# Kernel tuning notes

Measured on AMD Instinct MI355X. Metric: run time of the kernel, lower is better.

The kernel has to match this reference:

```python
import jax, jax.numpy as jnp
import numpy as np
import math
from jax import lax

B = 128; T = 1024; ENC = 768; H = 256; NMEL = 400
DC = 8; DK = 21; SK = 21; PL = 11

def _prior_np():
    # betabinom.pmf(arange(11), 10, 0.1, 0.9), then flipped (as in torch buffer)
    n = PL - 1; a = 0.1; b = 0.9; lg = math.lgamma
    lp = [lg(n + 1) - lg(k + 1) - lg(n - k + 1) + lg(k + a) + lg(n - k + b) - lg(n + a + b) + lg(a + b) - lg(a) - lg(b) for k in range(PL)]
    return np.exp(np.array(lp, dtype=np.float64))[::-1].copy().astype(np.float32)

def _gru(x, h, wih, whh, bih, bhh):
    # torch GRUCell gate order: r, z, n
    gi = x @ wih.T + bih
    gh = h @ whh.T + bhh
    ir, iz, inn = jnp.split(gi, 3, axis=-1)
    hr, hz, hn = jnp.split(gh, 3, axis=-1)
    r = jax.nn.sigmoid(ir + hr)
    z = jax.nn.sigmoid(iz + hz)
    n = jnp.tanh(inn + r * hn)
    return (1.0 - z) * n + z * h

def _dca(s, alpha, Ww, Wb, Vw, Fk, Uw, Tw, Tb, vw, P):
    Bn, Tn = alpha.shape
    dn = ('NCH', 'OIH', 'NCH')
    # causal prior convolution with flipped beta-binomial pmf
    ap = jnp.pad(alpha[:, None, :], ((0, 0), (0, 0), (PL - 1, 0)))
    p = lax.conv_general_dilated(ap, P.reshape(1, 1, PL), (1,), 'VALID', dimension_numbers=dn)[:, 0, :]
    p = jnp.log(jnp.clip(p, 1e-6))
    # dynamic filters: one [DC, DK] kernel per batch element
    G = jnp.tanh(s @ Ww.T + Wb) @ Vw.T            # [B, DC*DK]
    gk = G.reshape(Bn * DC, 1, DK)
    pad = (DK - 1) // 2
    g = lax.conv_general_dilated(alpha[None, :, :], gk, (1,), [(pad, pad)], dimension_numbers=dn, feature_group_count=Bn)
    g = g.reshape(Bn, DC, Tn).transpose(0, 2, 1)  # [B, T, DC]
    spad = (SK - 1) // 2
    f = lax.conv_general_dilated(alpha[:, None, :], Fk, (1,), [(spad, spad)], dimension_numbers=dn).transpose(0, 2, 1)  # [B, T, SC]
    e = (jnp.tanh(f @ Uw.T + g @ Tw.T + Tb) @ vw.T)[..., 0] + p
    return jax.nn.softmax(e, axis=-1)

def setup_inputs() -> dict:
    key = jax.random.key(0)
    ks = jax.random.split(key, 32)
    s = 0.05
    def nrm(k, shape, sc=s):
        return jax.random.normal(k, shape, dtype=jnp.float32) * sc
    a0 = jax.random.uniform(ks[0], (B, T), dtype=jnp.float32)
    prev_attention = a0 / jnp.sum(a0, axis=-1, keepdims=True)
    return {
        'encoder_outputs': nrm(ks[1], (B, T, ENC), 1.0),
        'prev_frame': nrm(ks[2], (B, NMEL), 1.0),
        'prev_attention': prev_attention,
        'decoder_cell_state': nrm(ks[3], (B, ENC), 1.0),
        'h_att': nrm(ks[4], (B, H), 1.0),
        'h1': nrm(ks[5], (B, H), 1.0),
        'h2': nrm(ks[6], (B, H), 1.0),
        'pre_w1': nrm(ks[7], (H, NMEL)), 'pre_b1': jnp.zeros((H,), jnp.float32),
        'pre_w2': nrm(ks[8], (H // 2, H)), 'pre_b2': jnp.zeros((H // 2,), jnp.float32),
        'dca_Ww': nrm(ks[9], (128, H)), 'dca_Wb': jnp.zeros((128,), jnp.float32),
        'dca_Vw': nrm(ks[10], (DC * DK, 128)),
        'dca_Fk': nrm(ks[11], (DC, 1, SK)),
        'dca_Uw': nrm(ks[12], (128, DC)),
        'dca_Tw': nrm(ks[13], (128, DC)), 'dca_Tb': jnp.zeros((128,), jnp.float32),
        'dca_vw': nrm(ks[14], (1, 128)),
        'att_wih': nrm(ks[15], (3 * H, ENC + H // 2)), 'att_whh': nrm(ks[16], (3 * H, H)),
        'att_bih': jnp.zeros((3 * H,), jnp.float32), 'att_bhh': jnp.zeros((3 * H,), jnp.float32),
        'lin_w': nrm(ks[17], (H, ENC + H)), 'lin_b': jnp.zeros((H,), jnp.float32),
        'r1_wih': nrm(ks[18], (3 * H, H)), 'r1_whh': nrm(ks[19], (3 * H, H)),
        'r1_bih': jnp.zeros((3 * H,), jnp.float32), 'r1_bhh': jnp.zeros((3 * H,), jnp.float32),
        'r2_wih': nrm(ks[20], (3 * H, H)), 'r2_whh': nrm(ks[21], (3 * H, H)),
        'r2_bih': jnp.zeros((3 * H,), jnp.float32), 'r2_bhh': jnp.zeros((3 * H,), jnp.float32),
        'proj_w': nrm(ks[22], (NMEL, H)), 'proj_b': jnp.zeros((NMEL,), jnp.float32),
        'P': jnp.asarray(_prior_np()),
    }

def reference(encoder_outputs, prev_frame, prev_attention, decoder_cell_state, h_att, h1, h2, pre_w1, pre_b1, pre_w2, pre_b2, dca_Ww, dca_Wb, dca_Vw, dca_Fk, dca_Uw, dca_Tw, dca_Tb, dca_vw, att_wih, att_whh, att_bih, att_bhh, lin_w, lin_b, r1_wih, r1_whh, r1_bih, r1_bhh, r2_wih, r2_whh, r2_bih, r2_bhh, proj_w, proj_b, P):
    # pre-net (eval: dropout = identity)
    o = jax.nn.relu(prev_frame @ pre_w1.T + pre_b1)
    o = jax.nn.relu(o @ pre_w2.T + pre_b2)
    h_att_n = _gru(jnp.concatenate([decoder_cell_state, o], axis=-1), h_att, att_wih, att_whh, att_bih, att_bhh)
    alpha = _dca(h_att_n, prev_attention, dca_Ww, dca_Wb, dca_Vw, dca_Fk, dca_Uw, dca_Tw, dca_Tb, dca_vw, P)
    dcs = jnp.einsum('bt,bte->be', alpha, encoder_outputs)
    x = jnp.concatenate([dcs, h_att_n], axis=-1) @ lin_w.T + lin_b
    h1n = _gru(x, h1, r1_wih, r1_whh, r1_bih, r1_bhh)
    x = x + h1n
    h2n = _gru(x, h2, r2_wih, r2_whh, r2_bih, r2_bhh)
    x = x + h2n
    out = (x @ proj_w.T + proj_b).reshape(-1, 80, 5)
    return (out, alpha, dcs, h_att_n, h1n, h2n)
```

## Files before the change

### kernel.cpp

```cpp
#include <hip/hip_runtime.h>

typedef unsigned short u16;
typedef unsigned int u32;

#define NB   128
#define NT   1024
#define NENC 768
#define NH   256
#define NMELS 400

constexpr int OFF_FLAG  = 0;
constexpr int OFF_HATTN = 16;
constexpr int OFF_G     = OFF_HATTN + NB*NH;
constexpr int OFF_ALPHA = OFF_G + NB*168;
constexpr int OFF_DCS   = OFF_ALPHA + NB*NT;
constexpr int OFF_UT    = OFF_DCS + NB*NENC;
constexpr int OFF_TBF   = OFF_UT + 2048;
constexpr int OFF_VWF   = OFF_TBF + 128;
constexpr int OFF_FKF   = OFF_VWF + 128;
constexpr int OFF_PF    = OFF_FKF + 168;

constexpr int OUT_MEL   = 0;
constexpr int OUT_ALPHA = OUT_MEL + NB*NMELS;
constexpr int OUT_DCS   = OUT_ALPHA + NB*NT;
constexpr int OUT_HATT  = OUT_DCS + NB*NENC;
constexpr int OUT_H1    = OUT_HATT + NB*NH;
constexpr int OUT_H2    = OUT_H1 + NB*NH;

__device__ __forceinline__ float bfd(u16 u){ u32 x = ((u32)u) << 16; return __builtin_bit_cast(float, x); }
__device__ __forceinline__ float bflo(u32 u){ return __builtin_bit_cast(float, u << 16); }
__device__ __forceinline__ float bfhi(u32 u){ return __builtin_bit_cast(float, u & 0xffff0000u); }
__device__ __forceinline__ u16 f2bf(float f){
  u32 x = __builtin_bit_cast(u32, f);
  u32 r = x + 0x7fffu + ((x >> 16) & 1u);
  return (u16)(r >> 16);
}
__device__ __forceinline__ float sigm(float x){ return 1.f / (1.f + __expf(-x)); }
__device__ __forceinline__ float tanh_(float x){
  float e = __expf(2.f * x);
  return 1.f - 2.f / (e + 1.f);
}

template<int M> __device__ __forceinline__ float ld1(const void* p, size_t i){
  if constexpr (M) return bfd(((const u16*)p)[i]);
  else return ((const float*)p)[i];
}
template<int M> __device__ __forceinline__ float2 ldpair(const void* p, size_t k2){
  if constexpr (M){ u32 u = ((const u32*)p)[k2]; float2 r; r.x = bflo(u); r.y = bfhi(u); return r; }
  else return ((const float2*)p)[k2];
}
template<int M> __device__ __forceinline__ void st1(void* p, size_t i, float v){
  if constexpr (M) ((u16*)p)[i] = f2bf(v);
  else ((float*)p)[i] = v;
}

template<int M, int K>
__device__ __forceinline__ float gru_unit(const float* xs, const float* hs,
    const void* wih, const void* whh, const void* bih, const void* bhh, int j){
  float ir = ld1<M>(bih, j), iz = ld1<M>(bih, 256 + j), in_ = ld1<M>(bih, 512 + j);
  {
    size_t r0 = (size_t)j * (K / 2), z0 = (size_t)(256 + j) * (K / 2), n0 = (size_t)(512 + j) * (K / 2);
    #pragma unroll 4
    for (int k2 = 0; k2 < K / 2; k2++){
      float x0 = xs[2 * k2], x1 = xs[2 * k2 + 1];
      float2 wr = ldpair<M>(wih, r0 + k2);
      float2 wz = ldpair<M>(wih, z0 + k2);
      float2 wn = ldpair<M>(wih, n0 + k2);
      ir = fmaf(x0, wr.x, fmaf(x1, wr.y, ir));
      iz = fmaf(x0, wz.x, fmaf(x1, wz.y, iz));
      in_ = fmaf(x0, wn.x, fmaf(x1, wn.y, in_));
    }
  }
  float hr = ld1<M>(bhh, j), hz = ld1<M>(bhh, 256 + j), hn = ld1<M>(bhh, 512 + j);
  {
    size_t r0 = (size_t)j * 128, z0 = (size_t)(256 + j) * 128, n0 = (size_t)(512 + j) * 128;
    #pragma unroll 4
    for (int k2 = 0; k2 < 128; k2++){
      float h0 = hs[2 * k2], h1 = hs[2 * k2 + 1];
      float2 wr = ldpair<M>(whh, r0 + k2);
      float2 wz = ldpair<M>(whh, z0 + k2);
      float2 wn = ldpair<M>(whh, n0 + k2);
      hr = fmaf(h0, wr.x, fmaf(h1, wr.y, hr));
      hz = fmaf(h0, wz.x, fmaf(h1, wz.y, hz));
      hn = fmaf(h0, wn.x, fmaf(h1, wn.y, hn));
    }
  }
  float r = sigm(ir + hr), z = sigm(iz + hz);
  float n = tanh_(in_ + r * hn);
  return (1.f - z) * n + z * hs[j];
}

template<int M>
__device__ __forceinline__ void prep_body(const void* Uw, const void* Tw, const void* Tb,
    const void* vw, const void* Fk, const void* P, float* ws, int j){
  for (int i = j; i < 2048; i += 256){
    int m = i >> 4, c = i & 15;
    ws[OFF_UT + i] = (c < 8) ? ld1<M>(Uw, m * 8 + c) : ld1<M>(Tw, m * 8 + (c - 8));
  }
  if (j < 128){ ws[OFF_TBF + j] = ld1<M>(Tb, j); ws[OFF_VWF + j] = ld1<M>(vw, j); }
  if (j < 168) ws[OFF_FKF + j] = ld1<M>(Fk, j);
  if (j < 11)  ws[OFF_PF + j]  = ld1<M>(P, j);
}

__global__ void prep_kernel(const void* enc, const void* Uw, const void* Tw, const void* Tb,
                            const void* vw, const void* Fk, const void* P, float* ws){
  int j = threadIdx.x;
  __shared__ int cnt;
  if (j == 0) cnt = 0;
  __syncthreads();
  int c = 0;
  const u32* ep = (const u32*)enc;
  for (int i = j; i < 1024; i += 256){
    u32 w = ep[i] & 0xffffu;
    int ex = (int)((w >> 7) & 0xff);
    if (ex >= 0xC0) c++;
  }
  if (c) atomicAdd(&cnt, c);
  __syncthreads();
  int mode = (cnt > 8) ? 0 : 1;
  if (j == 0) ((int*)ws)[OFF_FLAG] = mode;
  if (mode) prep_body<1>(Uw, Tw, Tb, vw, Fk, P, ws, j);
  else      prep_body<0>(Uw, Tw, Tb, vw, Fk, P, ws, j);
}

template<int M>
__device__ __forceinline__ void head_body(const void* prev_frame, const void* dcs_state,
    const void* h_att, const void* pre_w1, const void* pre_b1, const void* pre_w2, const void* pre_b2,
    const void* att_wih, const void* att_whh, const void* att_bih, const void* att_bhh,
    const void* Ww, const void* Wb, const void* Vw,
    float* ws, void* out, float* sm){
  float* pf = sm;
  float* o1 = sm + 400;
  float* xc = sm + 656;
  float* hv = sm + 1552;
  float* hn = sm + 1808;
  float* t1 = sm + 2064;
  int b = blockIdx.x, j = threadIdx.x;
  for (int k = j; k < NMELS; k += 256) pf[k] = ld1<M>(prev_frame, (size_t)b * NMELS + k);
  for (int k = j; k < 768; k += 256)   xc[k] = ld1<M>(dcs_state, (size_t)b * 768 + k);
  hv[j] = ld1<M>(h_att, (size_t)b * 256 + j);
  __syncthreads();
  {
    float a = ld1<M>(pre_b1, j);
    size_t w0 = (size_t)j * 200;
    #pragma unroll 4
    for (int k2 = 0; k2 < 200; k2++){
      float2 w = ldpair<M>(pre_w1, w0 + k2);
      a = fmaf(pf[2 * k2], w.x, fmaf(pf[2 * k2 + 1], w.y, a));
    }
    o1[j] = fmaxf(a, 0.f);
  }
  __syncthreads();
  if (j < 128){
    float a = ld1<M>(pre_b2, j);
    size_t w0 = (size_t)j * 128;
    #pragma unroll 4
    for (int k2 = 0; k2 < 128; k2++){
      float2 w = ldpair<M>(pre_w2, w0 + k2);
      a = fmaf(o1[2 * k2], w.x, fmaf(o1[2 * k2 + 1], w.y, a));
    }
    xc[768 + j] = fmaxf(a, 0.f);
  }
  __syncthreads();
  float hnew = gru_unit<M, 896>(xc, hv, att_wih, att_whh, att_bih, att_bhh, j);
  hn[j] = hnew;
  ws[OFF_HATTN + b * 256 + j] = hnew;
  st1<M>(out, OUT_HATT + (size_t)b * 256 + j, hnew);
  __syncthreads();
  if (j < 128){
    float a = ld1<M>(Wb, j);
    size_t w0 = (size_t)j * 128;
    #pragma unroll 4
    for (int k2 = 0; k2 < 128; k2++){
      float2 w = ldpair<M>(Ww, w0 + k2);
      a = fmaf(hn[2 * k2], w.x, fmaf(hn[2 * k2 + 1], w.y, a));
    }
    t1[j] = tanh_(a);
  }
  __syncthreads();
  if (j < 168){
    float a = 0.f;
    size_t w0 = (size_t)j * 64;
    #pragma unroll 4
    for (int k2 = 0; k2 < 64; k2++){
      float2 w = ldpair<M>(Vw, w0 + k2);
      a = fmaf(t1[2 * k2], w.x, fmaf(t1[2 * k2 + 1], w.y, a));
    }
    ws[OFF_G + b * 168 + j] = a;
  }
}

__global__ __launch_bounds__(256)
void head_kernel(const void* prev_frame, const void* dcs_state, const void* h_att,
    const void* pre_w1, const void* pre_b1, const void* pre_w2, const void* pre_b2,
    const void* att_wih, const void* att_whh, const void* att_bih, const void* att_bhh,
    const void* Ww, const void* Wb, const void* Vw, float* ws, void* out){
  __shared__ float sm[2192];
  if (((const int*)ws)[OFF_FLAG])
    head_body<1>(prev_frame, dcs_state, h_att, pre_w1, pre_b1, pre_w2, pre_b2,
                 att_wih, att_whh, att_bih, att_bhh, Ww, Wb, Vw, ws, out, sm);
  else
    head_body<0>(prev_frame, dcs_state, h_att, pre_w1, pre_b1, pre_w2, pre_b2,
                 att_wih, att_whh, att_bih, att_bhh, Ww, Wb, Vw, ws, out, sm);
}

template<int M>
__device__ __forceinline__ void dca_body(const void* prev_att, float* ws, void* out, float* sm){
  float* apad = sm;
  float* red  = sm + 1044;
  float* bc   = sm + 1060;
  int b = blockIdx.x, t = threadIdx.x;
  if (t < NENC) ws[OFF_DCS + b * NENC + t] = 0.f;
  if (t < 10){ apad[t] = 0.f; apad[NT + 10 + t] = 0.f; }
  apad[10 + t] = ld1<M>(prev_att, (size_t)b * NT + t);
  __syncthreads();
  float ap[21];
  #pragma unroll
  for (int k = 0; k < 21; k++) ap[k] = apad[t + k];
  const float* Pw = ws + OFF_PF;
  float pv = 0.f;
  #pragma unroll
  for (int jj = 0; jj < 11; jj++) pv = fmaf(Pw[jj], ap[jj], pv);
  pv = __logf(fmaxf(pv, 1e-6f));
  const float* Fw = ws + OFF_FKF;
  const float* Gw = ws + OFF_G + b * 168;
  float fg[16];
  #pragma unroll
  for (int c = 0; c < 8; c++){
    float fa = 0.f, ga = 0.f;
    #pragma unroll
    for (int k = 0; k < 21; k++){
      fa = fmaf(Fw[c * 21 + k], ap[k], fa);
      ga = fmaf(Gw[c * 21 + k], ap[k], ga);
    }
    fg[c] = fa; fg[8 + c] = ga;
  }
  const float* UT  = ws + OFF_UT;
  const float* Tbf = ws + OFF_TBF;
  const float* vwf = ws + OFF_VWF;
  float e = pv;
  #pragma unroll 4
  for (int m = 0; m < 128; m++){
    float h = Tbf[m];
    #pragma unroll
    for (int c = 0; c < 16; c++) h = fmaf(UT[m * 16 + c], fg[c], h);
    e = fmaf(vwf[m], tanh_(h), e);
  }
  float mx = e;
  #pragma unroll
  for (int off = 1; off < 64; off <<= 1) mx = fmaxf(mx, __shfl_xor(mx, off));
  if ((t & 63) == 0) red[t >> 6] = mx;
  __syncthreads();
  if (t == 0){ float m2 = red[0]; for (int i = 1; i < 16; i++) m2 = fmaxf(m2, red[i]); bc[0] = m2; }
  __syncthreads();
  float ex = __expf(e - bc[0]);
  float smv = ex;
  #pragma unroll
  for (int off = 1; off < 64; off <<= 1) smv += __shfl_xor(smv, off);
  if ((t & 63) == 0) red[t >> 6] = smv;
  __syncthreads();
  if (t == 0){ float s2 = 0.f; for (int i = 0; i < 16; i++) s2 += red[i]; bc[1] = s2; }
  __syncthreads();
  float al = ex / bc[1];
  ws[OFF_ALPHA + b * NT + t] = al;
  st1<M>(out, OUT_ALPHA + (size_t)b * NT + t, al);
}

__global__ __launch_bounds__(1024)
void dca_e_kernel(const void* prev_att, float* ws, void* out){
  __shared__ float sm[1062];
  if (((const int*)ws)[OFF_FLAG]) dca_body<1>(prev_att, ws, out, sm);
  else                            dca_body<0>(prev_att, ws, out, sm);
}

template<int M>
__device__ __forceinline__ void dcs_body(const void* enc, float* ws, float* sA){
  int ch = blockIdx.x, b = blockIdx.y, j = threadIdx.x;
  int t0 = ch * 128;
  if (j < 128) sA[j] = ws[OFF_ALPHA + b * NT + t0 + j];
  __syncthreads();
  float a0 = 0.f, a1 = 0.f, a2 = 0.f, a3 = 0.f;
  size_t wbase = ((size_t)(b * NT + t0) * NENC) / 2 + 2 * j;
  #pragma unroll 4
  for (int tl = 0; tl < 128; tl++){
    float a = sA[tl];
    float2 p0 = ldpair<M>(enc, wbase + (size_t)tl * (NENC / 2));
    float2 p1 = ldpair<M>(enc, wbase + (size_t)tl * (NENC / 2) + 1);
    a0 = fmaf(a, p0.x, a0);
    a1 = fmaf(a, p0.y, a1);
    a2 = fmaf(a, p1.x, a2);
    a3 = fmaf(a, p1.y, a3);
  }
  float* o = ws + OFF_DCS + (size_t)b * NENC + 4 * j;
  atomicAdd(o + 0, a0);
  atomicAdd(o + 1, a1);
  atomicAdd(o + 2, a2);
  atomicAdd(o + 3, a3);
}

__global__ __launch_bounds__(192)
void dcs_kernel(const void* enc, float* ws){
  __shared__ float sA[128];
  if (((const int*)ws)[OFF_FLAG]) dcs_body<1>(enc, ws, sA);
  else                            dcs_body<0>(enc, ws, sA);
}

template<int M>
__device__ __forceinline__ void tail_body(float* ws,
    const void* lin_w, const void* lin_b,
    const void* r1_wih, const void* r1_whh, const void* r1_bih, const void* r1_bhh,
    const void* r2_wih, const void* r2_whh, const void* r2_bih, const void* r2_bhh,
    const void* proj_w, const void* proj_b,
    const void* h1_in, const void* h2_in, void* out, float* sm){
  float* xc  = sm;
  float* sx  = sm + 1024;
  float* sx2 = sm + 1280;
  float* sx3 = sm + 1536;
  float* h1s = sm + 1792;
  float* h2s = sm + 2048;
  int b = blockIdx.x, j = threadIdx.x;
  for (int k = j; k < NENC; k += 256){
    float s = ws[OFF_DCS + (size_t)b * NENC + k];
    xc[k] = s;
    st1<M>(out, OUT_DCS + (size_t)b * NENC + k, s);
  }
  xc[768 + j] = ws[OFF_HATTN + b * 256 + j];
  h1s[j] = ld1<M>(h1_in, (size_t)b * 256 + j);
  h2s[j] = ld1<M>(h2_in, (size_t)b * 256 + j);
  __syncthreads();
  {
    float a = ld1<M>(lin_b, j);
    size_t w0 = (size_t)j * 512;
    #pragma unroll 4
    for (int k2 = 0; k2 < 512; k2++){
      float2 w = ldpair<M>(lin_w, w0 + k2);
      a = fmaf(xc[2 * k2], w.x, fmaf(xc[2 * k2 + 1], w.y, a));
    }
    sx[j] = a;
  }
  __syncthreads();
  float h1n = gru_unit<M, 256>(sx, h1s, r1_wih, r1_whh, r1_bih, r1_bhh, j);
  st1<M>(out, OUT_H1 + (size_t)b * 256 + j, h1n);
  sx2[j] = sx[j] + h1n;
  __syncthreads();
  float h2n = gru_unit<M, 256>(sx2, h2s, r2_wih, r2_whh, r2_bih, r2_bhh, j);
  st1<M>(out, OUT_H2 + (size_t)b * 256 + j, h2n);
  sx3[j] = sx2[j] + h2n;
  __syncthreads();
  for (int o = j; o < NMELS; o += 256){
    float a = ld1<M>(proj_b, o);
    size_t w0 = (size_t)o * 128;
    #pragma unroll 4
    for (int k2 = 0; k2 < 128; k2++){
      float2 w = ldpair<M>(proj_w, w0 + k2);
      a = fmaf(sx3[2 * k2], w.x, fmaf(sx3[2 * k2 + 1], w.y, a));
    }
    st1<M>(out, OUT_MEL + (size_t)b * NMELS + o, a);
  }
}

__global__ __launch_bounds__(256)
void tail_kernel(float* ws,
    const void* lin_w, const void* lin_b,
    const void* r1_wih, const void* r1_whh, const void* r1_bih, const void* r1_bhh,
    const void* r2_wih, const void* r2_whh, const void* r2_bih, const void* r2_bhh,
    const void* proj_w, const void* proj_b,
    const void* h1_in, const void* h2_in, void* out){
  __shared__ float sm[2304];
  if (((const int*)ws)[OFF_FLAG])
    tail_body<1>(ws, lin_w, lin_b, r1_wih, r1_whh, r1_bih, r1_bhh,
                 r2_wih, r2_whh, r2_bih, r2_bhh, proj_w, proj_b, h1_in, h2_in, out, sm);
  else
    tail_body<0>(ws, lin_w, lin_b, r1_wih, r1_whh, r1_bih, r1_bhh,
                 r2_wih, r2_whh, r2_bih, r2_bhh, proj_w, proj_b, h1_in, h2_in, out, sm);
}

extern "C" void kernel_launch(void* const* d_in, const int* in_sizes, int n_in,
                              void* d_out, int out_size, void* d_ws, size_t ws_size,
                              hipStream_t stream){
  (void)in_sizes; (void)n_in; (void)out_size; (void)ws_size;
  const void* enc       = d_in[0];
  const void* prev_frame= d_in[1];
  const void* prev_att  = d_in[2];
  const void* dcs_state = d_in[3];
  const void* h_att     = d_in[4];
  const void* h1        = d_in[5];
  const void* h2        = d_in[6];
  const void* pre_w1    = d_in[7];
  const void* pre_b1    = d_in[8];
  const void* pre_w2    = d_in[9];
  const void* pre_b2    = d_in[10];
  const void* dca_Ww    = d_in[11];
  const void* dca_Wb    = d_in[12];
  const void* dca_Vw    = d_in[13];
  const void* dca_Fk    = d_in[14];
  const void* dca_Uw    = d_in[15];
  const void* dca_Tw    = d_in[16];
  const void* dca_Tb    = d_in[17];
  const void* dca_vw    = d_in[18];
  const void* att_wih   = d_in[19];
  const void* att_whh   = d_in[20];
  const void* att_bih   = d_in[21];
  const void* att_bhh   = d_in[22];
  const void* lin_w     = d_in[23];
  const void* lin_b     = d_in[24];
  const void* r1_wih    = d_in[25];
  const void* r1_whh    = d_in[26];
  const void* r1_bih    = d_in[27];
  const void* r1_bhh    = d_in[28];
  const void* r2_wih    = d_in[29];
  const void* r2_whh    = d_in[30];
  const void* r2_bih    = d_in[31];
  const void* r2_bhh    = d_in[32];
  const void* proj_w    = d_in[33];
  const void* proj_b    = d_in[34];
  const void* P         = d_in[35];
  float* ws = (float*)d_ws;
  void* out = d_out;

  prep_kernel<<<1, 256, 0, stream>>>(enc, dca_Uw, dca_Tw, dca_Tb, dca_vw, dca_Fk, P, ws);
  head_kernel<<<NB, 256, 0, stream>>>(prev_frame, dcs_state, h_att,
      pre_w1, pre_b1, pre_w2, pre_b2,
      att_wih, att_whh, att_bih, att_bhh,
      dca_Ww, dca_Wb, dca_Vw, ws, out);
  dca_e_kernel<<<NB, 1024, 0, stream>>>(prev_att, ws, out);
  dcs_kernel<<<dim3(8, NB), 192, 0, stream>>>(enc, ws);
  tail_kernel<<<NB, 256, 0, stream>>>(ws, lin_w, lin_b,
      r1_wih, r1_whh, r1_bih, r1_bhh,
      r2_wih, r2_whh, r2_bih, r2_bhh,
      proj_w, proj_b, h1, h2, out);
}
```

Before: 991.5 us.

## Switch matvecs to warp-per-row coalesced dot products with shuffle reductions

```diff
diff --git a/kernel.cpp b/kernel.cpp
--- a/kernel.cpp
+++ b/kernel.cpp
@@ -49,44 +49,51 @@
   if constexpr (M){ u32 u = ((const u32*)p)[k2]; float2 r; r.x = bflo(u); r.y = bfhi(u); return r; }
   else return ((const float2*)p)[k2];
 }
+template<int M> __device__ __forceinline__ float4 ldquad(const void* p, size_t q){
+  if constexpr (M){
+    uint2 u = ((const uint2*)p)[q];
+    float4 r; r.x = bflo(u.x); r.y = bfhi(u.x); r.z = bflo(u.y); r.w = bfhi(u.y); return r;
+  } else return ((const float4*)p)[q];
+}
 template<int M> __device__ __forceinline__ void st1(void* p, size_t i, float v){
   if constexpr (M) ((u16*)p)[i] = f2bf(v);
   else ((float*)p)[i] = v;
 }
 
-template<int M, int K>
-__device__ __forceinline__ float gru_unit(const float* xs, const float* hs,
-    const void* wih, const void* whh, const void* bih, const void* bhh, int j){
-  float ir = ld1<M>(bih, j), iz = ld1<M>(bih, 256 + j), in_ = ld1<M>(bih, 512 + j);
-  {
-    size_t r0 = (size_t)j * (K / 2), z0 = (size_t)(256 + j) * (K / 2), n0 = (size_t)(512 + j) * (K / 2);
-    #pragma unroll 4
-    for (int k2 = 0; k2 < K / 2; k2++){
-      float x0 = xs[2 * k2], x1 = xs[2 * k2 + 1];
-      float2 wr = ldpair<M>(wih, r0 + k2);
-      float2 wz = ldpair<M>(wih, z0 + k2);
-      float2 wn = ldpair<M>(wih, n0 + k2);
-      ir = fmaf(x0, wr.x, fmaf(x1, wr.y, ir));
-      iz = fmaf(x0, wz.x, fmaf(x1, wz.y, iz));
-      in_ = fmaf(x0, wn.x, fmaf(x1, wn.y, in_));
+__device__ __forceinline__ float wred(float v){
+  #pragma unroll
+  for (int off = 1; off < 64; off <<= 1) v += __shfl_xor(v, off);
+  return v;
+}
+
+template<int M, int K2>
+__device__ __forceinline__ float wdot(const void* W, size_t row, const float* x, int l){
+  float a = 0.f;
+  #pragma unroll
+  for (int p0 = 0; p0 < K2; p0 += 64){
+    int p = p0 + l;
+    if (K2 % 64 == 0 || p < K2){
+      float2 w = ldpair<M>(W, row * K2 + p);
+      a = fmaf(x[2 * p], w.x, fmaf(x[2 * p + 1], w.y, a));
     }
   }
-  float hr = ld1<M>(bhh, j), hz = ld1<M>(bhh, 256 + j), hn = ld1<M>(bhh, 512 + j);
-  {
-    size_t r0 = (size_t)j * 128, z0 = (size_t)(256 + j) * 128, n0 = (size_t)(512 + j) * 128;
-    #pragma unroll 4
-    for (int k2 = 0; k2 < 128; k2++){
-      float h0 = hs[2 * k2], h1 = hs[2 * k2 + 1];
-      float2 wr = ldpair<M>(whh, r0 + k2);
-      float2 wz = ldpair<M>(whh, z0 + k2);
-      float2 wn = ldpair<M>(whh, n0 + k2);
-      hr = fmaf(h0, wr.x, fmaf(h1, wr.y, hr));
-      hz = fmaf(h0, wz.x, fmaf(h1, wz.y, hz));
-      hn = fmaf(h0, wn.x, fmaf(h1, wn.y, hn));
-    }
-  }
-  float r = sigm(ir + hr), z = sigm(iz + hz);
-  float n = tanh_(in_ + r * hn);
+  return a;
+}
+
+template<int M, int KX2>
+__device__ __forceinline__ float gru_wave(const float* xs, const float* hs,
+    const void* wih, const void* whh, const void* bih, const void* bhh, int j, int l){
+  float ir = wdot<M, KX2>(wih, j, xs, l);
+  float iz = wdot<M, KX2>(wih, 256 + j, xs, l);
+  float in_ = wdot<M, KX2>(wih, 512 + j, xs, l);
+  float hr = wdot<M, 128>(whh, j, hs, l);
+  float hz = wdot<M, 128>(whh, 256 + j, hs, l);
+  float hn = wdot<M, 128>(whh, 512 + j, hs, l);
+  ir = wred(ir); iz = wred(iz); in_ = wred(in_);
+  hr = wred(hr); hz = wred(hz); hn = wred(hn);
+  float r = sigm(ir + ld1<M>(bih, j) + hr + ld1<M>(bhh, j));
+  float z = sigm(iz + ld1<M>(bih, 256 + j) + hz + ld1<M>(bhh, 256 + j));
+  float n = tanh_(in_ + ld1<M>(bih, 512 + j) + r * (hn + ld1<M>(bhh, 512 + j)));
   return (1.f - z) * n + z * hs[j];
 }
 
@@ -135,58 +142,39 @@
   float* hv = sm + 1552;
   float* hn = sm + 1808;
   float* t1 = sm + 2064;
-  int b = blockIdx.x, j = threadIdx.x;
-  for (int k = j; k < NMELS; k += 256) pf[k] = ld1<M>(prev_frame, (size_t)b * NMELS + k);
-  for (int k = j; k < 768; k += 256)   xc[k] = ld1<M>(dcs_state, (size_t)b * 768 + k);
-  hv[j] = ld1<M>(h_att, (size_t)b * 256 + j);
-  __syncthreads();
-  {
-    float a = ld1<M>(pre_b1, j);
-    size_t w0 = (size_t)j * 200;
-    #pragma unroll 4
-    for (int k2 = 0; k2 < 200; k2++){
-      float2 w = ldpair<M>(pre_w1, w0 + k2);
-      a = fmaf(pf[2 * k2], w.x, fmaf(pf[2 * k2 + 1], w.y, a));
+  int b = blockIdx.x, tid = threadIdx.x;
+  int w = tid >> 6, l = tid & 63;
+  for (int p = tid; p < 200; p += 256){ float2 v = ldpair<M>(prev_frame, (size_t)b * 200 + p); pf[2*p] = v.x; pf[2*p+1] = v.y; }
+  for (int p = tid; p < 384; p += 256){ float2 v = ldpair<M>(dcs_state, (size_t)b * 384 + p); xc[2*p] = v.x; xc[2*p+1] = v.y; }
+  if (tid < 128){ float2 v = ldpair<M>(h_att, (size_t)b * 128 + tid); hv[2*tid] = v.x; hv[2*tid+1] = v.y; }
+  __syncthreads();
+  for (int j = w; j < 256; j += 4){
+    float a = wred(wdot<M, 200>(pre_w1, j, pf, l));
+    if (l == 0) o1[j] = fmaxf(a + ld1<M>(pre_b1, j), 0.f);
+  }
+  __syncthreads();
+  for (int j = w; j < 128; j += 4){
+    float a = wred(wdot<M, 128>(pre_w2, j, o1, l));
+    if (l == 0) xc[768 + j] = fmaxf(a + ld1<M>(pre_b2, j), 0.f);
+  }
+  __syncthreads();
+  for (int j = w; j < 256; j += 4){
+    float hnew = gru_wave<M, 448>(xc, hv, att_wih, att_whh, att_bih, att_bhh, j, l);
+    if (l == 0){
+      hn[j] = hnew;
+      ws[OFF_HATTN + b * 256 + j] = hnew;
     }
-    o1[j] = fmaxf(a, 0.f);
-  }
-  __syncthreads();
-  if (j < 128){
-    float a = ld1<M>(pre_b2, j);
-    size_t w0 = (size_t)j * 128;
-    #pragma unroll 4
-    for (int k2 = 0; k2 < 128; k2++){
-      float2 w = ldpair<M>(pre_w2, w0 + k2);
-      a = fmaf(o1[2 * k2], w.x, fmaf(o1[2 * k2 + 1], w.y, a));
-    }
-    xc[768 + j] = fmaxf(a, 0.f);
-  }
-  __syncthreads();
-  float hnew = gru_unit<M, 896>(xc, hv, att_wih, att_whh, att_bih, att_bhh, j);
-  hn[j] = hnew;
-  ws[OFF_HATTN + b * 256 + j] = hnew;
-  st1<M>(out, OUT_HATT + (size_t)b * 256 + j, hnew);
-  __syncthreads();
-  if (j < 128){
-    float a = ld1<M>(Wb, j);
-    size_t w0 = (size_t)j * 128;
-    #pragma unroll 4
-    for (int k2 = 0; k2 < 128; k2++){
-      float2 w = ldpair<M>(Ww, w0 + k2);
-      a = fmaf(hn[2 * k2], w.x, fmaf(hn[2 * k2 + 1], w.y, a));
-    }
-    t1[j] = tanh_(a);
-  }
-  __syncthreads();
-  if (j < 168){
-    float a = 0.f;
-    size_t w0 = (size_t)j * 64;
-    #pragma unroll 4
-    for (int k2 = 0; k2 < 64; k2++){
-      float2 w = ldpair<M>(Vw, w0 + k2);
-      a = fmaf(t1[2 * k2], w.x, fmaf(t1[2 * k2 + 1], w.y, a));
-    }
-    ws[OFF_G + b * 168 + j] = a;
+    if (l == 1) st1<M>(out, OUT_HATT + (size_t)b * 256 + j, hnew);
+  }
+  __syncthreads();
+  for (int j = w; j < 128; j += 4){
+    float a = wred(wdot<M, 128>(Ww, j, hn, l));
+    if (l == 0) t1[j] = tanh_(a + ld1<M>(Wb, j));
+  }
+  __syncthreads();
+  for (int j = w; j < 168; j += 4){
+    float a = wred(wdot<M, 64>(Vw, j, t1, l));
+    if (l == 0) ws[OFF_G + b * 168 + j] = a;
   }
 }
 
@@ -205,25 +193,26 @@
 }
 
 template<int M>
-__device__ __forceinline__ void dca_body(const void* prev_att, float* ws, void* out, float* sm){
+__device__ __forceinline__ void dca_body(const void* prev_att, const float* __restrict__ wsc,
+                                         float* ws, void* out, float* sm){
   float* apad = sm;
   float* red  = sm + 1044;
   float* bc   = sm + 1060;
   int b = blockIdx.x, t = threadIdx.x;
   if (t < NENC) ws[OFF_DCS + b * NENC + t] = 0.f;
   if (t < 10){ apad[t] = 0.f; apad[NT + 10 + t] = 0.f; }
-  apad[10 + t] = ld1<M>(prev_att, (size_t)b * NT + t);
+  if (t < 512){ float2 v = ldpair<M>(prev_att, (size_t)b * 512 + t); apad[10 + 2*t] = v.x; apad[10 + 2*t + 1] = v.y; }
   __syncthreads();
   float ap[21];
   #pragma unroll
   for (int k = 0; k < 21; k++) ap[k] = apad[t + k];
-  const float* Pw = ws + OFF_PF;
+  const float* Pw = wsc + OFF_PF;
   float pv = 0.f;
   #pragma unroll
   for (int jj = 0; jj < 11; jj++) pv = fmaf(Pw[jj], ap[jj], pv);
   pv = __logf(fmaxf(pv, 1e-6f));
-  const float* Fw = ws + OFF_FKF;
-  const float* Gw = ws + OFF_G + b * 168;
+  const float* Fw = wsc + OFF_FKF;
+  const float* Gw = wsc + OFF_G + b * 168;
   float fg[16];
   #pragma unroll
   for (int c = 0; c < 8; c++){
@@ -235,9 +224,9 @@
     }
     fg[c] = fa; fg[8 + c] = ga;
   }
-  const float* UT  = ws + OFF_UT;
-  const float* Tbf = ws + OFF_TBF;
-  const float* vwf = ws + OFF_VWF;
+  const float* UT  = wsc + OFF_UT;
+  const float* Tbf = wsc + OFF_TBF;
+  const float* vwf = wsc + OFF_VWF;
   float e = pv;
   #pragma unroll 4
   for (int m = 0; m < 128; m++){
@@ -269,8 +258,8 @@
 __global__ __launch_bounds__(1024)
 void dca_e_kernel(const void* prev_att, float* ws, void* out){
   __shared__ float sm[1062];
-  if (((const int*)ws)[OFF_FLAG]) dca_body<1>(prev_att, ws, out, sm);
-  else                            dca_body<0>(prev_att, ws, out, sm);
+  if (((const int*)ws)[OFF_FLAG]) dca_body<1>(prev_att, ws, ws, out, sm);
+  else                            dca_body<0>(prev_att, ws, ws, out, sm);
 }
 
 template<int M>
@@ -280,16 +269,15 @@
   if (j < 128) sA[j] = ws[OFF_ALPHA + b * NT + t0 + j];
   __syncthreads();
   float a0 = 0.f, a1 = 0.f, a2 = 0.f, a3 = 0.f;
-  size_t wbase = ((size_t)(b * NT + t0) * NENC) / 2 + 2 * j;
+  size_t qbase = (size_t)(b * NT + t0) * (NENC / 4) + j;
   #pragma unroll 4
   for (int tl = 0; tl < 128; tl++){
     float a = sA[tl];
-    float2 p0 = ldpair<M>(enc, wbase + (size_t)tl * (NENC / 2));
-    float2 p1 = ldpair<M>(enc, wbase + (size_t)tl * (NENC / 2) + 1);
-    a0 = fmaf(a, p0.x, a0);
-    a1 = fmaf(a, p0.y, a1);
-    a2 = fmaf(a, p1.x, a2);
-    a3 = fmaf(a, p1.y, a3);
+    float4 q = ldquad<M>(enc, qbase + (size_t)tl * (NENC / 4));
+    a0 = fmaf(a, q.x, a0);
+    a1 = fmaf(a, q.y, a1);
+    a2 = fmaf(a, q.z, a2);
+    a3 = fmaf(a, q.w, a3);
   }
   float* o = ws + OFF_DCS + (size_t)b * NENC + 4 * j;
   atomicAdd(o + 0, a0);
@@ -318,44 +306,39 @@
   float* sx3 = sm + 1536;
   float* h1s = sm + 1792;
   float* h2s = sm + 2048;
-  int b = blockIdx.x, j = threadIdx.x;
-  for (int k = j; k < NENC; k += 256){
+  int b = blockIdx.x, tid = threadIdx.x;
+  int w = tid >> 6, l = tid & 63;
+  for (int k = tid; k < NENC; k += 256){
     float s = ws[OFF_DCS + (size_t)b * NENC + k];
     xc[k] = s;
     st1<M>(out, OUT_DCS + (size_t)b * NENC + k, s);
   }
-  xc[768 + j] = ws[OFF_HATTN + b * 256 + j];
-  h1s[j] = ld1<M>(h1_in, (size_t)b * 256 + j);
-  h2s[j] = ld1<M>(h2_in, (size_t)b * 256 + j);
-  __syncthreads();
-  {
-    float a = ld1<M>(lin_b, j);
-    size_t w0 = (size_t)j * 512;
-    #pragma unroll 4
-    for (int k2 = 0; k2 < 512; k2++){
-      float2 w = ldpair<M>(lin_w, w0 + k2);
-      a = fmaf(xc[2 * k2], w.x, fmaf(xc[2 * k2 + 1], w.y, a));
-    }
-    sx[j] = a;
-  }
-  __syncthreads();
-  float h1n = gru_unit<M, 256>(sx, h1s, r1_wih, r1_whh, r1_bih, r1_bhh, j);
-  st1<M>(out, OUT_H1 + (size_t)b * 256 + j, h1n);
-  sx2[j] = sx[j] + h1n;
-  __syncthreads();
-  float h2n = gru_unit<M, 256>(sx2, h2s, r2_wih, r2_whh, r2_bih, r2_bhh, j);
-  st1<M>(out, OUT_H2 + (size_t)b * 256 + j, h2n);
-  sx3[j] = sx2[j] + h2n;
-  __syncthreads();
-  for (int o = j; o < NMELS; o += 256){
-    float a = ld1<M>(proj_b, o);
-    size_t w0 = (size_t)o * 128;
-    #pragma unroll 4
-    for (int k2 = 0; k2 < 128; k2++){
-      float2 w = ldpair<M>(proj_w, w0 + k2);
-      a = fmaf(sx3[2 * k2], w.x, fmaf(sx3[2 * k2 + 1], w.y, a));
-    }
-    st1<M>(out, OUT_MEL + (size_t)b * NMELS + o, a);
+  xc[768 + tid] = ws[OFF_HATTN + b * 256 + tid];
+  if (tid < 128){
+    float2 v = ldpair<M>(h1_in, (size_t)b * 128 + tid); h1s[2*tid] = v.x; h1s[2*tid+1] = v.y;
+    float2 u = ldpair<M>(h2_in, (size_t)b * 128 + tid); h2s[2*tid] = u.x; h2s[2*tid+1] = u.y;
+  }
+  __syncthreads();
+  for (int j = w; j < 256; j += 4){
+    float a = wred(wdot<M, 512>(lin_w, j, xc, l));
+    if (l == 0) sx[j] = a + ld1<M>(lin_b, j);
+  }
+  __syncthreads();
+  for (int j = w; j < 256; j += 4){
+    float h1n = gru_wave<M, 128>(sx, h1s, r1_wih, r1_whh, r1_bih, r1_bhh, j, l);
+    if (l == 0) sx2[j] = sx[j] + h1n;
+    if (l == 1) st1<M>(out, OUT_H1 + (size_t)b * 256 + j, h1n);
+  }
+  __syncthreads();
+  for (int j = w; j < 256; j += 4){
+    float h2n = gru_wave<M, 128>(sx2, h2s, r2_wih, r2_whh, r2_bih, r2_bhh, j, l);
+    if (l == 0) sx3[j] = sx2[j] + h2n;
+    if (l == 1) st1<M>(out, OUT_H2 + (size_t)b * 256 + j, h2n);
+  }
+  __syncthreads();
+  for (int j = w; j < 400; j += 4){
+    float a = wred(wdot<M, 128>(proj_w, j, sx3, l));
+    if (l == 0) st1<M>(out, OUT_MEL + (size_t)b * NMELS + j, a + ld1<M>(proj_b, j));
   }
 }
 
```

Result: slower. 1.168 ms (+17.8%).
